# Performance work log

Measured on AMD Instinct MI355X. Metric: run time of the kernel, lower is better.

Reference implementation:

```python
import jax, jax.numpy as jnp
import numpy as np

NT, NC, NM = 500_000, 100_000, 20_000   # transaction / client / merchant node counts
E = 500_000                              # edges per relation
IN, EMB, HID, OUT = 128, 64, 64, 2


def _lin_init(k, fan_in, fan_out):
    s = 1.0 / np.sqrt(fan_in)
    k1, k2 = jax.random.split(k)
    W = jax.random.uniform(k1, (fan_in, fan_out), jnp.float32, -s, s)
    b = jax.random.uniform(k2, (fan_out,), jnp.float32, -s, s)
    return W, b


def setup_inputs() -> dict:
    key = jax.random.key(0)
    ks = jax.random.split(key, 24)
    it = iter(range(24))
    d = {}
    d["features"] = jax.random.normal(ks[next(it)], (NT, IN), jnp.float32)
    d["emb_client"] = jax.random.normal(ks[next(it)], (NC, EMB), jnp.float32)
    d["emb_merchant"] = jax.random.normal(ks[next(it)], (NM, EMB), jnp.float32)
    for name, n_src, n_dst in [("c2t", NC, NT), ("m2t", NM, NT), ("t2c", NT, NC), ("t2m", NT, NM)]:
        d[f"src_{name}"] = jax.random.randint(ks[next(it)], (E,), 0, n_src)
        d[f"dst_{name}"] = jax.random.randint(ks[next(it)], (E,), 0, n_dst)
    # per-etype input size: in_size if src==transaction else embedding_size
    in0 = {"c2t": EMB, "m2t": EMB, "t2c": IN, "t2m": IN}
    for e in ["c2t", "m2t", "t2c", "t2m"]:
        d[f"W0_{e}"], d[f"b0_{e}"] = _lin_init(ks[next(it)], in0[e], HID)
        d[f"W1_{e}"], d[f"b1_{e}"] = _lin_init(ks[next(it)], HID, HID)
    d["Wf"], d["bf"] = _lin_init(ks[next(it)], HID, OUT)
    return d


def _seg_mean(msg, dst, n):
    # copy_u 'm' + mean reduce; zero in-degree dst nodes get 0 (DGL semantics)
    s = jax.ops.segment_sum(msg, dst, num_segments=n)
    cnt = jax.ops.segment_sum(jnp.ones((msg.shape[0], 1), msg.dtype), dst, num_segments=n)
    return s / jnp.maximum(cnt, 1.0)


def reference(features, emb_client, emb_merchant,
              src_c2t, dst_c2t, src_m2t, dst_m2t,
              src_t2c, dst_t2c, src_t2m, dst_t2m,
              W0_c2t, b0_c2t, W1_c2t, b1_c2t,
              W0_m2t, b0_m2t, W1_m2t, b1_m2t,
              W0_t2c, b0_t2c, W1_t2c, b1_t2c,
              W0_t2m, b0_t2m, W1_t2m, b1_t2m,
              Wf, bf):
    sizes = {"t": NT, "c": NC, "m": NM}
    edges = {"c2t": ("c", "t", src_c2t, dst_c2t),
             "m2t": ("m", "t", src_m2t, dst_m2t),
             "t2c": ("t", "c", src_t2c, dst_t2c),
             "t2m": ("t", "m", src_t2m, dst_t2m)}

    def rgcn_layer(h, W, b):
        acc = {}
        for e, (s, t, src, dst) in edges.items():
            wh = h[s] @ W[e] + b[e]                 # per-relation Linear on src nodes
            m = _seg_mean(wh[src], dst, sizes[t])   # gather + segment-mean
            acc[t] = acc.get(t, 0.0) + m            # cross-relation 'sum'
        return acc

    W0 = {"c2t": W0_c2t, "m2t": W0_m2t, "t2c": W0_t2c, "t2m": W0_t2m}
    b0 = {"c2t": b0_c2t, "m2t": b0_m2t, "t2c": b0_t2c, "t2m": b0_t2m}
    W1 = {"c2t": W1_c2t, "m2t": W1_m2t, "t2c": W1_t2c, "t2m": W1_t2m}
    b1 = {"c2t": b1_c2t, "m2t": b1_m2t, "t2c": b1_t2c, "t2m": b1_t2m}

    h = {"t": features, "c": emb_client, "m": emb_merchant}
    h = rgcn_layer(h, W0, b0)
    h = {k: jax.nn.leaky_relu(v) for k, v in h.items()}  # applied before layer i!=0
    h = rgcn_layer(h, W1, b1)
    return h["t"] @ Wf + bf                          # final Linear on target ntype
```

## Files before the change

### kernel.cpp

```cpp
#include <hip/hip_runtime.h>
#include <stdint.h>

#define NT 500000
#define NC 100000
#define NM 20000
#define NE 500000

__global__ __launch_bounds__(256) void weq_kernel(const float* __restrict__ W1c,
                                                  const float* __restrict__ b1c,
                                                  const float* __restrict__ W1m,
                                                  const float* __restrict__ b1m,
                                                  const float* __restrict__ Wf,
                                                  float* __restrict__ WeqC,
                                                  float* __restrict__ WeqM,
                                                  float* __restrict__ beq) {
    int t = threadIdx.x;
    if (t < 128) {
        int k = t >> 1, o = t & 1;
        float s = 0.0f;
        for (int j = 0; j < 64; j++) s += W1c[k * 64 + j] * Wf[j * 2 + o];
        WeqC[k * 2 + o] = s;
    } else {
        int k = (t - 128) >> 1, o = t & 1;
        float s = 0.0f;
        for (int j = 0; j < 64; j++) s += W1m[k * 64 + j] * Wf[j * 2 + o];
        WeqM[k * 2 + o] = s;
    }
    if (t < 4) {
        const float* b = (t < 2) ? b1c : b1m;
        int o = t & 1;
        float s = 0.0f;
        for (int j = 0; j < 64; j++) s += b[j] * Wf[j * 2 + o];
        beq[t] = s;
    }
}

__global__ __launch_bounds__(256) void hist_both(const int* __restrict__ dstC,
                                                 const int* __restrict__ dstM,
                                                 int* __restrict__ cntC,
                                                 int* __restrict__ cntM) {
    int e = blockIdx.x * 256 + threadIdx.x;
    if (e < NE) {
        atomicAdd(&cntC[dstC[e]], 1);
    } else {
        e -= NE;
        if (e < NE) atomicAdd(&cntM[dstM[e]], 1);
    }
}

__global__ __launch_bounds__(256) void blocksum_both(const int* __restrict__ cC,
                                                     const int* __restrict__ cM,
                                                     int* __restrict__ blkC,
                                                     int* __restrict__ blkM) {
    int b = blockIdx.x;
    const int* counts; int* blk; int n, bb;
    if (b < 98) { counts = cC; blk = blkC; n = NC; bb = b; }
    else        { counts = cM; blk = blkM; n = NM; bb = b - 98; }
    int tid = threadIdx.x;
    int base = bb * 1024 + tid * 4;
    int s = 0;
#pragma unroll
    for (int j = 0; j < 4; j++) { int i = base + j; if (i < n) s += counts[i]; }
    for (int off = 32; off; off >>= 1) s += __shfl_down(s, off, 64);
    __shared__ int wsum[4];
    if ((tid & 63) == 0) wsum[tid >> 6] = s;
    __syncthreads();
    if (tid == 0) blk[bb] = wsum[0] + wsum[1] + wsum[2] + wsum[3];
}

__global__ __launch_bounds__(256) void scanblk_both(int* __restrict__ blkC,
                                                    int* __restrict__ blkM) {
    int* blk; int nb;
    if (blockIdx.x == 0) { blk = blkC; nb = 98; }
    else                 { blk = blkM; nb = 20; }
    __shared__ int sh[256];
    int tid = threadIdx.x;
    int v = tid < nb ? blk[tid] : 0;
    sh[tid] = v; __syncthreads();
    for (int off = 1; off < 256; off <<= 1) {
        int t = (tid >= off) ? sh[tid - off] : 0;
        __syncthreads();
        sh[tid] += t;
        __syncthreads();
    }
    if (tid < nb) blk[tid] = sh[tid] - v;
}

__global__ __launch_bounds__(256) void scanfinal_both(int* __restrict__ rowPtrC,
                                                      int* __restrict__ cursorC,
                                                      const int* __restrict__ blkC,
                                                      int* __restrict__ rowPtrM,
                                                      int* __restrict__ cursorM,
                                                      const int* __restrict__ blkM) {
    int b = blockIdx.x;
    int* rowPtr; int* cursor; const int* blkOff; int n, bb;
    if (b < 98) { rowPtr = rowPtrC; cursor = cursorC; blkOff = blkC; n = NC; bb = b; }
    else        { rowPtr = rowPtrM; cursor = cursorM; blkOff = blkM; n = NM; bb = b - 98; }
    int tid = threadIdx.x, lane = tid & 63, wv = tid >> 6;
    int base = bb * 1024 + tid * 4;
    int c[4];
#pragma unroll
    for (int j = 0; j < 4; j++) { int i = base + j; c[j] = (i < n) ? rowPtr[i] : 0; }
    int t = c[0] + c[1] + c[2] + c[3];
    int incl = t;
    for (int off = 1; off < 64; off <<= 1) {
        int u = __shfl_up(incl, off, 64);
        if (lane >= off) incl += u;
    }
    int lexcl = incl - t;
    __shared__ int wsum[4], woff[4];
    if (lane == 63) wsum[wv] = incl;
    __syncthreads();
    if (tid == 0) { int a = 0; for (int w = 0; w < 4; w++) { woff[w] = a; a += wsum[w]; } }
    __syncthreads();
    int e = blkOff[bb] + woff[wv] + lexcl;
#pragma unroll
    for (int j = 0; j < 4; j++) {
        int i = base + j;
        if (i < n) {
            rowPtr[i] = e;
            cursor[i] = e;
            if (i == n - 1) rowPtr[n] = e + c[j];
        }
        e += c[j];
    }
}

__global__ __launch_bounds__(256) void scatter_both(const int* __restrict__ srcC,
                                                    const int* __restrict__ dstC,
                                                    int* __restrict__ cursorC,
                                                    int* __restrict__ eidxC,
                                                    const int* __restrict__ srcM,
                                                    const int* __restrict__ dstM,
                                                    int* __restrict__ cursorM,
                                                    int* __restrict__ eidxM) {
    int e = blockIdx.x * 256 + threadIdx.x;
    if (e < NE) {
        int pos = atomicAdd(&cursorC[dstC[e]], 1);
        eidxC[pos] = srcC[e];
    } else {
        e -= NE;
        if (e < NE) {
            int pos = atomicAdd(&cursorM[dstM[e]], 1);
            eidxM[pos] = srcM[e];
        }
    }
}

__global__ __launch_bounds__(256) void agg_csr(const float* __restrict__ feat,
                                               const int* __restrict__ rowPtr,
                                               const int* __restrict__ eidx,
                                               float* __restrict__ sum,
                                               int base, int nNodes) {
    int gw = (blockIdx.x * 256 + threadIdx.x) >> 6;
    if (gw >= nNodes) return;
    int lane = threadIdx.x & 63;
    int half = lane >> 5;
    int c4 = (lane & 31) * 4;
    int d = base + gw;
    int s0 = rowPtr[d], s1 = rowPtr[d + 1];
    float a0 = 0.f, a1 = 0.f, a2 = 0.f, a3 = 0.f;
    int i = s0;
    for (; i + 1 < s1; i += 2) {
        int s = eidx[i + half];
        const float4 v = *(const float4*)(feat + (size_t)s * 128 + c4);
        a0 += v.x; a1 += v.y; a2 += v.z; a3 += v.w;
    }
    if (i < s1 && half == 0) {
        int s = eidx[i];
        const float4 v = *(const float4*)(feat + (size_t)s * 128 + c4);
        a0 += v.x; a1 += v.y; a2 += v.z; a3 += v.w;
    }
    a0 += __shfl_xor(a0, 32, 64);
    a1 += __shfl_xor(a1, 32, 64);
    a2 += __shfl_xor(a2, 32, 64);
    a3 += __shfl_xor(a3, 32, 64);
    if (half == 0) {
        float4 o; o.x = a0; o.y = a1; o.z = a2; o.w = a3;
        *(float4*)(sum + (size_t)gw * 128 + c4) = o;
    }
}

__global__ __launch_bounds__(256) void h1proj(const float* __restrict__ sum,
                                              const int* __restrict__ rowPtrB,
                                              const float* __restrict__ W0,
                                              const float* __restrict__ b0,
                                              const float* __restrict__ Weq,
                                              float* __restrict__ p, int n) {
    __shared__ float Ws[128 * 64];
    __shared__ float sums[32 * 128];
    int tid = threadIdx.x;
    int base = blockIdx.x * 32;
    {
        const float4* W4 = (const float4*)W0;
        float4* Ws4 = (float4*)Ws;
        for (int i = tid; i < 128 * 64 / 4; i += 256) Ws4[i] = W4[i];
    }
    {
        const float4* S4 = (const float4*)sum;
        float4* s4 = (float4*)sums;
        for (int i = tid; i < 32 * 128 / 4; i += 256) {
            int r = i >> 5;
            int row = base + r;
            float4 v;
            if (row < n) v = S4[(size_t)base * 32 + i];
            else { v.x = v.y = v.z = v.w = 0.0f; }
            s4[i] = v;
        }
    }
    __syncthreads();
    int col = tid & 63, wv = tid >> 6;
    float acc[8];
#pragma unroll
    for (int r = 0; r < 8; r++) acc[r] = 0.0f;
    const float* srow = &sums[wv * 8 * 128];
    for (int k = 0; k < 128; k += 4) {
        float w0_ = Ws[(k + 0) * 64 + col];
        float w1_ = Ws[(k + 1) * 64 + col];
        float w2_ = Ws[(k + 2) * 64 + col];
        float w3_ = Ws[(k + 3) * 64 + col];
#pragma unroll
        for (int r = 0; r < 8; r++) {
            const float4 s = *(const float4*)&srow[r * 128 + k];
            acc[r] += s.x * w0_ + s.y * w1_ + s.z * w2_ + s.w * w3_;
        }
    }
    float b0c = b0[col];
    float wq0 = Weq[col * 2 + 0], wq1 = Weq[col * 2 + 1];
#pragma unroll
    for (int r = 0; r < 8; r++) {
        int row = base + wv * 8 + r;
        int cn = 0;
        if (row < n) cn = rowPtrB[row + 1] - rowPtrB[row];
        float h = 0.0f;
        if (cn > 0) {
            float v = acc[r] / (float)cn + b0c;
            h = v > 0.0f ? v : 0.01f * v;
        }
        float p0 = h * wq0, p1 = h * wq1;
#pragma unroll
        for (int off = 32; off; off >>= 1) {
            p0 += __shfl_down(p0, off, 64);
            p1 += __shfl_down(p1, off, 64);
        }
        if (col == 0 && row < n) {
            p[(size_t)row * 2 + 0] = p0;
            p[(size_t)row * 2 + 1] = p1;
        }
    }
}

__global__ __launch_bounds__(256) void agg2_both(const float* __restrict__ pC,
                                                 const int* __restrict__ srcC,
                                                 const int* __restrict__ dstC,
                                                 float* __restrict__ accC,
                                                 float* __restrict__ cntC,
                                                 const float* __restrict__ pM,
                                                 const int* __restrict__ srcM,
                                                 const int* __restrict__ dstM,
                                                 float* __restrict__ accM,
                                                 float* __restrict__ cntM) {
    int e = blockIdx.x * 256 + threadIdx.x;
    const float* p; const int* src; const int* dst; float* acc; float* cnt;
    if (e < NE) { p = pC; src = srcC; dst = dstC; acc = accC; cnt = cntC; }
    else {
        e -= NE;
        if (e >= NE) return;
        p = pM; src = srcM; dst = dstM; acc = accM; cnt = cntM;
    }
    int s = src[e], d = dst[e];
    const float2 v = *(const float2*)(p + (size_t)s * 2);
    atomicAdd(acc + (size_t)d * 2 + 0, v.x);
    atomicAdd(acc + (size_t)d * 2 + 1, v.y);
    atomicAdd(cnt + d, 1.0f);
}

__global__ __launch_bounds__(256) void final_kernel(const float* __restrict__ accC,
                                                    const float* __restrict__ cntC,
                                                    const float* __restrict__ accM,
                                                    const float* __restrict__ cntM,
                                                    const float* __restrict__ beq,
                                                    const float* __restrict__ bfv,
                                                    float* __restrict__ out) {
    int i = blockIdx.x * 256 + threadIdx.x;
    if (i >= NT) return;
    float r0 = bfv[0], r1 = bfv[1];
    float cc = cntC[i], cm = cntM[i];
    if (cc > 0.0f) {
        float inv = 1.0f / cc;
        r0 += accC[(size_t)i * 2 + 0] * inv + beq[0];
        r1 += accC[(size_t)i * 2 + 1] * inv + beq[1];
    }
    if (cm > 0.0f) {
        float inv = 1.0f / cm;
        r0 += accM[(size_t)i * 2 + 0] * inv + beq[2];
        r1 += accM[(size_t)i * 2 + 1] * inv + beq[3];
    }
    float2 o; o.x = r0; o.y = r1;
    *(float2*)(out + (size_t)i * 2) = o;
}

extern "C" void kernel_launch(void* const* d_in, const int* in_sizes, int n_in,
                              void* d_out, int out_size, void* d_ws, size_t ws_size,
                              hipStream_t stream) {
    const float* feat = (const float*)d_in[0];
    const int* src_c2t = (const int*)d_in[3];
    const int* dst_c2t = (const int*)d_in[4];
    const int* src_m2t = (const int*)d_in[5];
    const int* dst_m2t = (const int*)d_in[6];
    const int* src_t2c = (const int*)d_in[7];
    const int* dst_t2c = (const int*)d_in[8];
    const int* src_t2m = (const int*)d_in[9];
    const int* dst_t2m = (const int*)d_in[10];
    const float* W1_c2t = (const float*)d_in[13];
    const float* b1_c2t = (const float*)d_in[14];
    const float* W1_m2t = (const float*)d_in[17];
    const float* b1_m2t = (const float*)d_in[18];
    const float* W0_t2c = (const float*)d_in[19];
    const float* b0_t2c = (const float*)d_in[20];
    const float* W0_t2m = (const float*)d_in[23];
    const float* b0_t2m = (const float*)d_in[24];
    const float* Wf  = (const float*)d_in[27];
    const float* bfv = (const float*)d_in[28];

    char* ws = (char*)d_ws;
    float* SUM     = (float*)(ws + 0);
    int*   rowPtrC = (int*)(ws + 25600000);
    int*   rowPtrM = (int*)(ws + 26000016);
    int*   cursorC = (int*)(ws + 26080032);
    int*   cursorM = (int*)(ws + 26480032);
    int*   eidxC   = (int*)(ws + 26560032);
    int*   eidxM   = (int*)(ws + 28560032);
    float* pC      = (float*)(ws + 30560032);
    float* pM      = (float*)(ws + 31360032);
    float* WeqC    = (float*)(ws + 31520032);
    float* WeqM    = (float*)(ws + 31520544);
    float* beq     = (float*)(ws + 31521056);
    int*   blkC    = (int*)(ws + 31521088);
    int*   blkM    = (int*)(ws + 31521600);
    float* accC    = (float*)(ws + 31522112);
    float* cntCT   = (float*)(ws + 35522112);
    float* accM    = (float*)(ws + 37522112);
    float* cntMT   = (float*)(ws + 41522112);

    hipMemsetAsync(rowPtrC, 0, 480032, stream);
    hipMemsetAsync(accC, 0, 12000000, stream);

    weq_kernel<<<1, 256, 0, stream>>>(W1_c2t, b1_c2t, W1_m2t, b1_m2t, Wf, WeqC, WeqM, beq);

    hist_both<<<3907, 256, 0, stream>>>(dst_t2c, dst_t2m, rowPtrC, rowPtrM);
    blocksum_both<<<118, 256, 0, stream>>>(rowPtrC, rowPtrM, blkC, blkM);
    scanblk_both<<<2, 256, 0, stream>>>(blkC, blkM);
    scanfinal_both<<<118, 256, 0, stream>>>(rowPtrC, cursorC, blkC, rowPtrM, cursorM, blkM);
    scatter_both<<<3907, 256, 0, stream>>>(src_t2c, dst_t2c, cursorC, eidxC,
                                           src_t2m, dst_t2m, cursorM, eidxM);

    agg_csr<<<12500, 256, 0, stream>>>(feat, rowPtrC, eidxC, SUM, 0, 50000);
    h1proj<<<1563, 256, 0, stream>>>(SUM, rowPtrC, W0_t2c, b0_t2c, WeqC, pC, 50000);
    agg_csr<<<12500, 256, 0, stream>>>(feat, rowPtrC, eidxC, SUM, 50000, 50000);
    h1proj<<<1563, 256, 0, stream>>>(SUM, rowPtrC + 50000, W0_t2c, b0_t2c, WeqC, pC + 100000, 50000);
    agg_csr<<<5000, 256, 0, stream>>>(feat, rowPtrM, eidxM, SUM, 0, 20000);
    h1proj<<<625, 256, 0, stream>>>(SUM, rowPtrM, W0_t2m, b0_t2m, WeqM, pM, 20000);

    agg2_both<<<3907, 256, 0, stream>>>(pC, src_c2t, dst_c2t, accC, cntCT,
                                        pM, src_m2t, dst_m2t, accM, cntMT);
    final_kernel<<<1954, 256, 0, stream>>>(accC, cntCT, accM, cntMT, beq, bfv, (float*)d_out);
}
```

Measured before the change: 849.2 us.

## Replace atomic scatter for second-layer aggregation with CSR gather fused into final

```diff
diff --git a/kernel.cpp b/kernel.cpp
--- a/kernel.cpp
+++ b/kernel.cpp
@@ -35,27 +35,37 @@
     }
 }
 
-__global__ __launch_bounds__(256) void hist_both(const int* __restrict__ dstC,
-                                                 const int* __restrict__ dstM,
-                                                 int* __restrict__ cntC,
-                                                 int* __restrict__ cntM) {
-    int e = blockIdx.x * 256 + threadIdx.x;
-    if (e < NE) {
-        atomicAdd(&cntC[dstC[e]], 1);
-    } else {
-        e -= NE;
-        if (e < NE) atomicAdd(&cntM[dstM[e]], 1);
-    }
-}
-
-__global__ __launch_bounds__(256) void blocksum_both(const int* __restrict__ cC,
-                                                     const int* __restrict__ cM,
-                                                     int* __restrict__ blkC,
-                                                     int* __restrict__ blkM) {
+__global__ __launch_bounds__(256) void hist4(const int* __restrict__ dTC,
+                                             const int* __restrict__ dTM,
+                                             const int* __restrict__ dCT,
+                                             const int* __restrict__ dMT,
+                                             int* __restrict__ cC,
+                                             int* __restrict__ cM,
+                                             int* __restrict__ cTC,
+                                             int* __restrict__ cTM) {
+    int id = blockIdx.x * 256 + threadIdx.x;
+    int r = id / NE;
+    int e = id - r * NE;
+    if (r == 0)      atomicAdd(&cC[dTC[e]], 1);
+    else if (r == 1) atomicAdd(&cM[dTM[e]], 1);
+    else if (r == 2) atomicAdd(&cTC[dCT[e]], 1);
+    else if (r == 3) atomicAdd(&cTM[dMT[e]], 1);
+}
+
+__global__ __launch_bounds__(256) void blocksum4(const int* __restrict__ cC,
+                                                 const int* __restrict__ cM,
+                                                 const int* __restrict__ cTC,
+                                                 const int* __restrict__ cTM,
+                                                 int* __restrict__ blkC,
+                                                 int* __restrict__ blkM,
+                                                 int* __restrict__ blkTC,
+                                                 int* __restrict__ blkTM) {
     int b = blockIdx.x;
     const int* counts; int* blk; int n, bb;
-    if (b < 98) { counts = cC; blk = blkC; n = NC; bb = b; }
-    else        { counts = cM; blk = blkM; n = NM; bb = b - 98; }
+    if (b < 98)       { counts = cC;  blk = blkC;  n = NC; bb = b; }
+    else if (b < 118) { counts = cM;  blk = blkM;  n = NM; bb = b - 98; }
+    else if (b < 607) { counts = cTC; blk = blkTC; n = NT; bb = b - 118; }
+    else              { counts = cTM; blk = blkTM; n = NT; bb = b - 607; }
     int tid = threadIdx.x;
     int base = bb * 1024 + tid * 4;
     int s = 0;
@@ -68,34 +78,51 @@
     if (tid == 0) blk[bb] = wsum[0] + wsum[1] + wsum[2] + wsum[3];
 }
 
-__global__ __launch_bounds__(256) void scanblk_both(int* __restrict__ blkC,
-                                                    int* __restrict__ blkM) {
+__global__ __launch_bounds__(256) void scanblk4(int* __restrict__ blkC,
+                                                int* __restrict__ blkM,
+                                                int* __restrict__ blkTC,
+                                                int* __restrict__ blkTM) {
     int* blk; int nb;
-    if (blockIdx.x == 0) { blk = blkC; nb = 98; }
-    else                 { blk = blkM; nb = 20; }
-    __shared__ int sh[256];
+    if (blockIdx.x == 0)      { blk = blkC;  nb = 98; }
+    else if (blockIdx.x == 1) { blk = blkM;  nb = 20; }
+    else if (blockIdx.x == 2) { blk = blkTC; nb = 489; }
+    else                      { blk = blkTM; nb = 489; }
+    __shared__ int ps[256];
     int tid = threadIdx.x;
-    int v = tid < nb ? blk[tid] : 0;
-    sh[tid] = v; __syncthreads();
+    int i0 = 2 * tid, i1 = i0 + 1;
+    int a = (i0 < nb) ? blk[i0] : 0;
+    int b = (i1 < nb) ? blk[i1] : 0;
+    ps[tid] = a + b;
+    __syncthreads();
     for (int off = 1; off < 256; off <<= 1) {
-        int t = (tid >= off) ? sh[tid - off] : 0;
+        int t = (tid >= off) ? ps[tid - off] : 0;
         __syncthreads();
-        sh[tid] += t;
+        ps[tid] += t;
         __syncthreads();
     }
-    if (tid < nb) blk[tid] = sh[tid] - v;
-}
-
-__global__ __launch_bounds__(256) void scanfinal_both(int* __restrict__ rowPtrC,
-                                                      int* __restrict__ cursorC,
-                                                      const int* __restrict__ blkC,
-                                                      int* __restrict__ rowPtrM,
-                                                      int* __restrict__ cursorM,
-                                                      const int* __restrict__ blkM) {
+    int excl = ps[tid] - (a + b);
+    if (i0 < nb) blk[i0] = excl;
+    if (i1 < nb) blk[i1] = excl + a;
+}
+
+__global__ __launch_bounds__(256) void scanfinal4(int* __restrict__ rowPtrC,
+                                                  int* __restrict__ cursorC,
+                                                  const int* __restrict__ blkC,
+                                                  int* __restrict__ rowPtrM,
+                                                  int* __restrict__ cursorM,
+                                                  const int* __restrict__ blkM,
+                                                  int* __restrict__ rowPtrTC,
+                                                  int* __restrict__ cursorTC,
+                                                  const int* __restrict__ blkTC,
+                                                  int* __restrict__ rowPtrTM,
+                                                  int* __restrict__ cursorTM,
+                                                  const int* __restrict__ blkTM) {
     int b = blockIdx.x;
     int* rowPtr; int* cursor; const int* blkOff; int n, bb;
-    if (b < 98) { rowPtr = rowPtrC; cursor = cursorC; blkOff = blkC; n = NC; bb = b; }
-    else        { rowPtr = rowPtrM; cursor = cursorM; blkOff = blkM; n = NM; bb = b - 98; }
+    if (b < 98)       { rowPtr = rowPtrC;  cursor = cursorC;  blkOff = blkC;  n = NC; bb = b; }
+    else if (b < 118) { rowPtr = rowPtrM;  cursor = cursorM;  blkOff = blkM;  n = NM; bb = b - 98; }
+    else if (b < 607) { rowPtr = rowPtrTC; cursor = cursorTC; blkOff = blkTC; n = NT; bb = b - 118; }
+    else              { rowPtr = rowPtrTM; cursor = cursorTM; blkOff = blkTM; n = NT; bb = b - 607; }
     int tid = threadIdx.x, lane = tid & 63, wv = tid >> 6;
     int base = bb * 1024 + tid * 4;
     int c[4];
@@ -126,25 +153,29 @@
     }
 }
 
-__global__ __launch_bounds__(256) void scatter_both(const int* __restrict__ srcC,
-                                                    const int* __restrict__ dstC,
-                                                    int* __restrict__ cursorC,
-                                                    int* __restrict__ eidxC,
-                                                    const int* __restrict__ srcM,
-                                                    const int* __restrict__ dstM,
-                                                    int* __restrict__ cursorM,
-                                                    int* __restrict__ eidxM) {
-    int e = blockIdx.x * 256 + threadIdx.x;
-    if (e < NE) {
-        int pos = atomicAdd(&cursorC[dstC[e]], 1);
-        eidxC[pos] = srcC[e];
-    } else {
-        e -= NE;
-        if (e < NE) {
-            int pos = atomicAdd(&cursorM[dstM[e]], 1);
-            eidxM[pos] = srcM[e];
-        }
-    }
+__global__ __launch_bounds__(256) void scatter4(const int* __restrict__ sTC,
+                                                const int* __restrict__ dTC,
+                                                int* __restrict__ curC,
+                                                int* __restrict__ eidxC,
+                                                const int* __restrict__ sTM,
+                                                const int* __restrict__ dTM,
+                                                int* __restrict__ curM,
+                                                int* __restrict__ eidxM,
+                                                const int* __restrict__ sCT,
+                                                const int* __restrict__ dCT,
+                                                int* __restrict__ curTC,
+                                                int* __restrict__ eidxTC,
+                                                const int* __restrict__ sMT,
+                                                const int* __restrict__ dMT,
+                                                int* __restrict__ curTM,
+                                                int* __restrict__ eidxTM) {
+    int id = blockIdx.x * 256 + threadIdx.x;
+    int r = id / NE;
+    int e = id - r * NE;
+    if (r == 0)      { int p = atomicAdd(&curC[dTC[e]], 1);  eidxC[p]  = sTC[e]; }
+    else if (r == 1) { int p = atomicAdd(&curM[dTM[e]], 1);  eidxM[p]  = sTM[e]; }
+    else if (r == 2) { int p = atomicAdd(&curTC[dCT[e]], 1); eidxTC[p] = sCT[e]; }
+    else if (r == 3) { int p = atomicAdd(&curTM[dMT[e]], 1); eidxTM[p] = sMT[e]; }
 }
 
 __global__ __launch_bounds__(256) void agg_csr(const float* __restrict__ feat,
@@ -250,51 +281,45 @@
     }
 }
 
-__global__ __launch_bounds__(256) void agg2_both(const float* __restrict__ pC,
-                                                 const int* __restrict__ srcC,
-                                                 const int* __restrict__ dstC,
-                                                 float* __restrict__ accC,
-                                                 float* __restrict__ cntC,
-                                                 const float* __restrict__ pM,
-                                                 const int* __restrict__ srcM,
-                                                 const int* __restrict__ dstM,
-                                                 float* __restrict__ accM,
-                                                 float* __restrict__ cntM) {
-    int e = blockIdx.x * 256 + threadIdx.x;
-    const float* p; const int* src; const int* dst; float* acc; float* cnt;
-    if (e < NE) { p = pC; src = srcC; dst = dstC; acc = accC; cnt = cntC; }
-    else {
-        e -= NE;
-        if (e >= NE) return;
-        p = pM; src = srcM; dst = dstM; acc = accM; cnt = cntM;
-    }
-    int s = src[e], d = dst[e];
-    const float2 v = *(const float2*)(p + (size_t)s * 2);
-    atomicAdd(acc + (size_t)d * 2 + 0, v.x);
-    atomicAdd(acc + (size_t)d * 2 + 1, v.y);
-    atomicAdd(cnt + d, 1.0f);
-}
-
-__global__ __launch_bounds__(256) void final_kernel(const float* __restrict__ accC,
-                                                    const float* __restrict__ cntC,
-                                                    const float* __restrict__ accM,
-                                                    const float* __restrict__ cntM,
+__global__ __launch_bounds__(256) void gather_final(const float* __restrict__ pC,
+                                                    const int* __restrict__ rowPtrTC,
+                                                    const int* __restrict__ eidxTC,
+                                                    const float* __restrict__ pM,
+                                                    const int* __restrict__ rowPtrTM,
+                                                    const int* __restrict__ eidxTM,
                                                     const float* __restrict__ beq,
                                                     const float* __restrict__ bfv,
                                                     float* __restrict__ out) {
     int i = blockIdx.x * 256 + threadIdx.x;
     if (i >= NT) return;
     float r0 = bfv[0], r1 = bfv[1];
-    float cc = cntC[i], cm = cntM[i];
-    if (cc > 0.0f) {
-        float inv = 1.0f / cc;
-        r0 += accC[(size_t)i * 2 + 0] * inv + beq[0];
-        r1 += accC[(size_t)i * 2 + 1] * inv + beq[1];
-    }
-    if (cm > 0.0f) {
-        float inv = 1.0f / cm;
-        r0 += accM[(size_t)i * 2 + 0] * inv + beq[2];
-        r1 += accM[(size_t)i * 2 + 1] * inv + beq[3];
+    {
+        int s0 = rowPtrTC[i], s1 = rowPtrTC[i + 1];
+        if (s1 > s0) {
+            float a0 = 0.f, a1 = 0.f;
+            for (int e = s0; e < s1; e++) {
+                int s = eidxTC[e];
+                const float2 v = *(const float2*)(pC + (size_t)s * 2);
+                a0 += v.x; a1 += v.y;
+            }
+            float inv = 1.0f / (float)(s1 - s0);
+            r0 += a0 * inv + beq[0];
+            r1 += a1 * inv + beq[1];
+        }
+    }
+    {
+        int s0 = rowPtrTM[i], s1 = rowPtrTM[i + 1];
+        if (s1 > s0) {
+            float a0 = 0.f, a1 = 0.f;
+            for (int e = s0; e < s1; e++) {
+                int s = eidxTM[e];
+                const float2 v = *(const float2*)(pM + (size_t)s * 2);
+                a0 += v.x; a1 += v.y;
+            }
+            float inv = 1.0f / (float)(s1 - s0);
+            r0 += a0 * inv + beq[2];
+            r1 += a1 * inv + beq[3];
+        }
     }
     float2 o; o.x = r0; o.y = r1;
     *(float2*)(out + (size_t)i * 2) = o;
@@ -324,36 +349,46 @@
     const float* bfv = (const float*)d_in[28];
 
     char* ws = (char*)d_ws;
-    float* SUM     = (float*)(ws + 0);
-    int*   rowPtrC = (int*)(ws + 25600000);
-    int*   rowPtrM = (int*)(ws + 26000016);
-    int*   cursorC = (int*)(ws + 26080032);
-    int*   cursorM = (int*)(ws + 26480032);
-    int*   eidxC   = (int*)(ws + 26560032);
-    int*   eidxM   = (int*)(ws + 28560032);
-    float* pC      = (float*)(ws + 30560032);
-    float* pM      = (float*)(ws + 31360032);
-    float* WeqC    = (float*)(ws + 31520032);
-    float* WeqM    = (float*)(ws + 31520544);
-    float* beq     = (float*)(ws + 31521056);
-    int*   blkC    = (int*)(ws + 31521088);
-    int*   blkM    = (int*)(ws + 31521600);
-    float* accC    = (float*)(ws + 31522112);
-    float* cntCT   = (float*)(ws + 35522112);
-    float* accM    = (float*)(ws + 37522112);
-    float* cntMT   = (float*)(ws + 41522112);
-
-    hipMemsetAsync(rowPtrC, 0, 480032, stream);
-    hipMemsetAsync(accC, 0, 12000000, stream);
+    float* SUM      = (float*)(ws + 0);
+    int*   rowPtrC  = (int*)(ws + 25600000);
+    int*   rowPtrM  = (int*)(ws + 26000016);
+    int*   rowPtrTC = (int*)(ws + 26080032);
+    int*   rowPtrTM = (int*)(ws + 28080036);
+    int*   cursorC  = (int*)(ws + 30080040);
+    int*   cursorM  = (int*)(ws + 30480040);
+    int*   cursorTC = (int*)(ws + 30560040);
+    int*   cursorTM = (int*)(ws + 32560040);
+    int*   eidxC    = (int*)(ws + 34560040);
+    int*   eidxM    = (int*)(ws + 36560040);
+    int*   eidxTC   = (int*)(ws + 38560040);
+    int*   eidxTM   = (int*)(ws + 40560040);
+    float* pC       = (float*)(ws + 42560040);
+    float* pM       = (float*)(ws + 43360040);
+    float* WeqC     = (float*)(ws + 43520040);
+    float* WeqM     = (float*)(ws + 43520552);
+    float* beq      = (float*)(ws + 43521064);
+    int*   blkC     = (int*)(ws + 43521080);
+    int*   blkM     = (int*)(ws + 43521472);
+    int*   blkTC    = (int*)(ws + 43521552);
+    int*   blkTM    = (int*)(ws + 43523508);
+
+    hipMemsetAsync(rowPtrC, 0, 4480040, stream);
 
     weq_kernel<<<1, 256, 0, stream>>>(W1_c2t, b1_c2t, W1_m2t, b1_m2t, Wf, WeqC, WeqM, beq);
 
-    hist_both<<<3907, 256, 0, stream>>>(dst_t2c, dst_t2m, rowPtrC, rowPtrM);
-    blocksum_both<<<118, 256, 0, stream>>>(rowPtrC, rowPtrM, blkC, blkM);
-    scanblk_both<<<2, 256, 0, stream>>>(blkC, blkM);
-    scanfinal_both<<<118, 256, 0, stream>>>(rowPtrC, cursorC, blkC, rowPtrM, cursorM, blkM);
-    scatter_both<<<3907, 256, 0, stream>>>(src_t2c, dst_t2c, cursorC, eidxC,
-                                           src_t2m, dst_t2m, cursorM, eidxM);
+    hist4<<<7813, 256, 0, stream>>>(dst_t2c, dst_t2m, dst_c2t, dst_m2t,
+                                    rowPtrC, rowPtrM, rowPtrTC, rowPtrTM);
+    blocksum4<<<1096, 256, 0, stream>>>(rowPtrC, rowPtrM, rowPtrTC, rowPtrTM,
+                                        blkC, blkM, blkTC, blkTM);
+    scanblk4<<<4, 256, 0, stream>>>(blkC, blkM, blkTC, blkTM);
+    scanfinal4<<<1096, 256, 0, stream>>>(rowPtrC, cursorC, blkC,
+                                         rowPtrM, cursorM, blkM,
+                                         rowPtrTC, cursorTC, blkTC,
+                                         rowPtrTM, cursorTM, blkTM);
+    scatter4<<<7813, 256, 0, stream>>>(src_t2c, dst_t2c, cursorC, eidxC,
+                                       src_t2m, dst_t2m, cursorM, eidxM,
+                                       src_c2t, dst_c2t, cursorTC, eidxTC,
+                                       src_m2t, dst_m2t, cursorTM, eidxTM);
 
     agg_csr<<<12500, 256, 0, stream>>>(feat, rowPtrC, eidxC, SUM, 0, 50000);
     h1proj<<<1563, 256, 0, stream>>>(SUM, rowPtrC, W0_t2c, b0_t2c, WeqC, pC, 50000);
@@ -362,7 +397,7 @@
     agg_csr<<<5000, 256, 0, stream>>>(feat, rowPtrM, eidxM, SUM, 0, 20000);
     h1proj<<<625, 256, 0, stream>>>(SUM, rowPtrM, W0_t2m, b0_t2m, WeqM, pM, 20000);
 
-    agg2_both<<<3907, 256, 0, stream>>>(pC, src_c2t, dst_c2t, accC, cntCT,
-                                        pM, src_m2t, dst_m2t, accM, cntMT);
-    final_kernel<<<1954, 256, 0, stream>>>(accC, cntCT, accM, cntMT, beq, bfv, (float*)d_out);
-}
+    gather_final<<<1954, 256, 0, stream>>>(pC, rowPtrTC, eidxTC,
+                                           pM, rowPtrTM, eidxTM,
+                                           beq, bfv, (float*)d_out);
+}
```

Result: faster. 825.7 us (-2.8%).
